# Optimization experiments

Hardware: AMD Instinct MI355X
Metric: run time of the kernel (lower is better)

Reference implementation:

```python
import jax, jax.numpy as jnp
import numpy as np


def setup_inputs() -> dict:
    key = jax.random.key(0)
    k1, k2 = jax.random.split(key)
    B, T, F, S, C = 16, 1024, 8, 128, 256
    e_src = jax.random.normal(k1, (B, T, F, C), dtype=jnp.float32)
    d_src = jax.random.randint(k2, (B, S), 0, 16, dtype=jnp.int64)
    return {"e_src": e_src, "d_src": d_src}


def reference(e_src, d_src):
    # Ragged per-phone mean pooling (the nested python loop in FastSpeech2Pros.forward):
    # e_src: [B, T_mel, F, C]; d_src: [B, S] frame durations per phone.
    # For b in range(B//2): chunk e_src[b] along T by durations, mean over (time, freq),
    # zeros for empty chunks -> agg [B//2, S, C].
    B, T, F, C = e_src.shape
    Bh = B // 2
    S = d_src.shape[1]
    e = e_src[:Bh]                      # [Bh, T, F, C]
    d = d_src[:Bh].astype(jnp.int32)    # [Bh, S]

    # frame t belongs to phone i iff cumsum(d)[i-1] <= t < cumsum(d)[i]
    cum = jnp.cumsum(d, axis=1)                                   # [Bh, S]
    t = jnp.arange(T, dtype=jnp.int32)
    seg = jax.vmap(lambda c: jnp.searchsorted(c, t, side='right'))(cum)  # [Bh, T]
    seg = jnp.minimum(seg, S)           # frames beyond total duration -> overflow bucket S

    frame_sum = e.sum(axis=2)           # [Bh, T, C] (sum over freq dim)
    sums = jax.vmap(
        lambda fs, s: jax.ops.segment_sum(fs, s, num_segments=S + 1)
    )(frame_sum, seg)[:, :S]            # [Bh, S, C]

    counts = (d * F).astype(e.dtype)    # elements per ragged chunk = dur * F
    agg = jnp.where(counts[..., None] > 0,
                    sums / jnp.maximum(counts, 1.0)[..., None],
                    jnp.zeros((), e.dtype))
    return agg
```

## Files before the change

### kernel.cpp

```cpp
#include <hip/hip_runtime.h>

#define TT 1024
#define SS 128
#define FF 8
#define CC 256
#define BH 8
#define TB 8

__global__ __launch_bounds__(256) void zero_kernel(float4* __restrict__ out) {
    out[blockIdx.x * 256 + threadIdx.x] = make_float4(0.f, 0.f, 0.f, 0.f);
}

__device__ __forceinline__ void flush_seg(float* __restrict__ out, int b, int s,
                                          int d0, int d1, int lane, float4 acc) {
    int dsel = (s & 1) ? d1 : d0;
    int ds   = __shfl(dsel, s >> 1, 64);
    float inv = 1.0f / (float)(ds * FF);
    float* o = out + ((size_t)(b * SS + s) * CC) + lane * 4;
    unsafeAtomicAdd(o + 0, acc.x * inv);
    unsafeAtomicAdd(o + 1, acc.y * inv);
    unsafeAtomicAdd(o + 2, acc.z * inv);
    unsafeAtomicAdd(o + 3, acc.w * inv);
}

__global__ __launch_bounds__(256) void fused_kernel(const float* __restrict__ e,
                                                    const int* __restrict__ dsrc,
                                                    float* __restrict__ out) {
    int x    = blockIdx.x;
    int b    = blockIdx.y;
    int tid  = threadIdx.x;
    int lane = tid & 63;
    int q    = tid >> 6;

    int2 dd = ((const int2*)(dsrc + b * SS))[lane];
    int incl = dd.x + dd.y;
    #pragma unroll
    for (int off = 1; off < 64; off <<= 1) {
        int n = __shfl_up(incl, off, 64);
        if (lane >= off) incl += n;
    }
    int cumO = incl;
    int cumE = incl - dd.y;

    int tA = x * TB + 2 * q;
    int tB = tA + 1;
    int segA = __popcll(__ballot(cumE <= tA)) + __popcll(__ballot(cumO <= tA));
    int segB = __popcll(__ballot(cumE <= tB)) + __popcll(__ballot(cumO <= tB));
    bool vA = segA < SS;
    bool vB = segB < SS;

    const float4* e4 = (const float4*)e + (size_t)(b * TT + x * TB) * (FF * CC / 4);
    const float4* w4 = e4 + (16 * q) * 64 + lane;

    float4 sA = make_float4(0.f, 0.f, 0.f, 0.f);
    float4 sB = make_float4(0.f, 0.f, 0.f, 0.f);
    if (vA) {
        #pragma unroll
        for (int j = 0; j < 8; ++j) {
            float4 v = w4[j * 64];
            sA.x += v.x; sA.y += v.y; sA.z += v.z; sA.w += v.w;
        }
    }
    if (vB) {
        #pragma unroll
        for (int j = 8; j < 16; ++j) {
            float4 v = w4[j * 64];
            sB.x += v.x; sB.y += v.y; sB.z += v.z; sB.w += v.w;
        }
    }

    if (vA && vB && segA == segB) {
        sA.x += sB.x; sA.y += sB.y; sA.z += sB.z; sA.w += sB.w;
        flush_seg(out, b, segA, dd.x, dd.y, lane, sA);
    } else {
        if (vA) flush_seg(out, b, segA, dd.x, dd.y, lane, sA);
        if (vB) flush_seg(out, b, segB, dd.x, dd.y, lane, sB);
    }
}

extern "C" void kernel_launch(void* const* d_in, const int* in_sizes, int n_in,
                              void* d_out, int out_size, void* d_ws, size_t ws_size,
                              hipStream_t stream) {
    const float* e   = (const float*)d_in[0];
    const int*   d   = (const int*)d_in[1];
    float*       out = (float*)d_out;

    zero_kernel<<<dim3(BH * SS * CC / 4 / 256), 256, 0, stream>>>((float4*)out);
    fused_kernel<<<dim3(TT / TB, BH), 256, 0, stream>>>(e, d, out);
}
```

Before: 182.8 us.

## Parallelize over segments and channel chunks, drop atomics and zero kernel

Replaces the frame-parallel kernel, which flushed partial sums to the output with atomics after a separate zero-fill launch, with one kernel. Each 64-thread block owns one (segment, 32-channel chunk) pair and sums that segment's frames and frequencies directly. Partial sums are reduced across lanes with shuffles and written once with plain stores, removing the atomic traffic and the extra launch. The cost is load imbalance across segments of different lengths, small one-wave blocks, and 32-channel-wide strided reads per frame row.

```diff
diff --git a/kernel.cpp b/kernel.cpp
--- a/kernel.cpp
+++ b/kernel.cpp
@@ -5,32 +5,15 @@
 #define FF 8
 #define CC 256
 #define BH 8
-#define TB 8
 
-__global__ __launch_bounds__(256) void zero_kernel(float4* __restrict__ out) {
-    out[blockIdx.x * 256 + threadIdx.x] = make_float4(0.f, 0.f, 0.f, 0.f);
-}
-
-__device__ __forceinline__ void flush_seg(float* __restrict__ out, int b, int s,
-                                          int d0, int d1, int lane, float4 acc) {
-    int dsel = (s & 1) ? d1 : d0;
-    int ds   = __shfl(dsel, s >> 1, 64);
-    float inv = 1.0f / (float)(ds * FF);
-    float* o = out + ((size_t)(b * SS + s) * CC) + lane * 4;
-    unsafeAtomicAdd(o + 0, acc.x * inv);
-    unsafeAtomicAdd(o + 1, acc.y * inv);
-    unsafeAtomicAdd(o + 2, acc.z * inv);
-    unsafeAtomicAdd(o + 3, acc.w * inv);
-}
-
-__global__ __launch_bounds__(256) void fused_kernel(const float* __restrict__ e,
-                                                    const int* __restrict__ dsrc,
-                                                    float* __restrict__ out) {
+__global__ __launch_bounds__(64) void fused_kernel(const float* __restrict__ e,
+                                                   const int* __restrict__ dsrc,
+                                                   float* __restrict__ out) {
     int x    = blockIdx.x;
     int b    = blockIdx.y;
-    int tid  = threadIdx.x;
-    int lane = tid & 63;
-    int q    = tid >> 6;
+    int lane = threadIdx.x;
+    int s    = x >> 3;
+    int ce   = x & 7;
 
     int2 dd = ((const int2*)(dsrc + b * SS))[lane];
     int incl = dd.x + dd.y;
@@ -39,42 +22,52 @@
         int n = __shfl_up(incl, off, 64);
         if (lane >= off) incl += n;
     }
-    int cumO = incl;
-    int cumE = incl - dd.y;
+    int l  = s >> 1;
+    int iS = __shfl(incl, l, 64);
+    int xS = __shfl(dd.x, l, 64);
+    int yS = __shfl(dd.y, l, 64);
+    int end   = (s & 1) ? iS : (iS - yS);
+    int dS    = (s & 1) ? yS : xS;
+    int start = end - dS;
+    if (start > TT) start = TT;
+    if (end   > TT) end   = TT;
+    int K = (end - start) * FF;
 
-    int tA = x * TB + 2 * q;
-    int tB = tA + 1;
-    int segA = __popcll(__ballot(cumE <= tA)) + __popcll(__ballot(cumO <= tA));
-    int segB = __popcll(__ballot(cumE <= tB)) + __popcll(__ballot(cumO <= tB));
-    bool vA = segA < SS;
-    bool vB = segB < SS;
+    int r8 = lane >> 3;
+    int fi = lane & 7;
+    const float4* base = (const float4*)e
+        + (size_t)(b * TT + start) * (FF * CC / 4)
+        + ce * 8 + fi;
 
-    const float4* e4 = (const float4*)e + (size_t)(b * TT + x * TB) * (FF * CC / 4);
-    const float4* w4 = e4 + (16 * q) * 64 + lane;
-
-    float4 sA = make_float4(0.f, 0.f, 0.f, 0.f);
-    float4 sB = make_float4(0.f, 0.f, 0.f, 0.f);
-    if (vA) {
-        #pragma unroll
-        for (int j = 0; j < 8; ++j) {
-            float4 v = w4[j * 64];
-            sA.x += v.x; sA.y += v.y; sA.z += v.z; sA.w += v.w;
-        }
+    float4 acc = make_float4(0.f, 0.f, 0.f, 0.f);
+    int k = r8;
+    for (; k + 24 < K; k += 32) {
+        float4 v0 = base[(size_t)(k     ) * 64];
+        float4 v1 = base[(size_t)(k +  8) * 64];
+        float4 v2 = base[(size_t)(k + 16) * 64];
+        float4 v3 = base[(size_t)(k + 24) * 64];
+        acc.x += v0.x + v1.x + v2.x + v3.x;
+        acc.y += v0.y + v1.y + v2.y + v3.y;
+        acc.z += v0.z + v1.z + v2.z + v3.z;
+        acc.w += v0.w + v1.w + v2.w + v3.w;
     }
-    if (vB) {
-        #pragma unroll
-        for (int j = 8; j < 16; ++j) {
-            float4 v = w4[j * 64];
-            sB.x += v.x; sB.y += v.y; sB.z += v.z; sB.w += v.w;
-        }
+    for (; k < K; k += 8) {
+        float4 v = base[(size_t)k * 64];
+        acc.x += v.x; acc.y += v.y; acc.z += v.z; acc.w += v.w;
     }
 
-    if (vA && vB && segA == segB) {
-        sA.x += sB.x; sA.y += sB.y; sA.z += sB.z; sA.w += sB.w;
-        flush_seg(out, b, segA, dd.x, dd.y, lane, sA);
-    } else {
-        if (vA) flush_seg(out, b, segA, dd.x, dd.y, lane, sA);
-        if (vB) flush_seg(out, b, segB, dd.x, dd.y, lane, sB);
+    #pragma unroll
+    for (int m = 8; m < 64; m <<= 1) {
+        acc.x += __shfl_xor(acc.x, m, 64);
+        acc.y += __shfl_xor(acc.y, m, 64);
+        acc.z += __shfl_xor(acc.z, m, 64);
+        acc.w += __shfl_xor(acc.w, m, 64);
+    }
+
+    if (lane < 8) {
+        float inv = (dS > 0) ? 1.0f / (float)(dS * FF) : 0.0f;
+        float4 r = make_float4(acc.x * inv, acc.y * inv, acc.z * inv, acc.w * inv);
+        ((float4*)out)[(size_t)(b * SS + s) * 64 + ce * 8 + lane] = r;
     }
 }
 
@@ -85,6 +78,5 @@
     const int*   d   = (const int*)d_in[1];
     float*       out = (float*)d_out;
 
-    zero_kernel<<<dim3(BH * SS * CC / 4 / 256), 256, 0, stream>>>((float4*)out);
-    fused_kernel<<<dim3(TT / TB, BH), 256, 0, stream>>>(e, d, out);
+    fused_kernel<<<dim3(SS * 8, BH), 64, 0, stream>>>(e, d, out);
 }
```

Measured after the change: 174.9 us. 1.05x faster.
